# Kernel tuning notes

Hardware: AMD Instinct MI355X
Metric: run time of the kernel (lower is better)

## Reference

```python
import jax, jax.numpy as jnp
import numpy as np

B, N, D, H, FF = 4, 1024, 512, 8, 2048
DH = D // H
RPE_HID = 16
COORD_DIM = 2


def _ln(x, g, b, eps=1e-5):
    m = jnp.mean(x, axis=-1, keepdims=True)
    v = jnp.mean((x - m) ** 2, axis=-1, keepdims=True)
    return (x - m) * jax.lax.rsqrt(v + eps) * g + b


def setup_inputs() -> dict:
    key = jax.random.key(0)
    ks = jax.random.split(key, 20)
    s = 0.02
    inp = {
        "x": jax.random.normal(ks[0], (B, N, D), dtype=jnp.float32),
        "coords": jax.random.uniform(ks[1], (B, N, COORD_DIM), dtype=jnp.float32),
        # qkv + output projections
        "Wq": jax.random.normal(ks[2], (D, D), jnp.float32) * s,
        "bq": jnp.zeros((D,), jnp.float32),
        "Wk": jax.random.normal(ks[3], (D, D), jnp.float32) * s,
        "bk": jnp.zeros((D,), jnp.float32),
        "Wv": jax.random.normal(ks[4], (D, D), jnp.float32) * s,
        "bv": jnp.zeros((D,), jnp.float32),
        "Wo": jax.random.normal(ks[5], (D, D), jnp.float32) * s,
        "bo": jnp.zeros((D,), jnp.float32),
        # learned per-head logit scale (Swin-v2 style cosine attention)
        "logit_scale": jnp.full((H, 1, 1), np.log(10.0), jnp.float32),
        # absolute positional embedder PE: Linear(2 -> D)
        "W_pe": jax.random.normal(ks[6], (COORD_DIM, D), jnp.float32) * s,
        "b_pe": jnp.zeros((D,), jnp.float32),
        # relative positional embedder RPE: MLP(2 -> 16 -> H)
        "W_r1": jax.random.normal(ks[7], (COORD_DIM, RPE_HID), jnp.float32) * 0.5,
        "b_r1": jnp.zeros((RPE_HID,), jnp.float32),
        "W_r2": jax.random.normal(ks[8], (RPE_HID, H), jnp.float32) * 0.5,
        "b_r2": jnp.zeros((H,), jnp.float32),
        # layernorm params
        "g_peq": jnp.ones((D,), jnp.float32), "bt_peq": jnp.zeros((D,), jnp.float32),
        "g_pek": jnp.ones((D,), jnp.float32), "bt_pek": jnp.zeros((D,), jnp.float32),
        "g2": jnp.ones((D,), jnp.float32), "bt2": jnp.zeros((D,), jnp.float32),
        "g3": jnp.ones((D,), jnp.float32), "bt3": jnp.zeros((D,), jnp.float32),
        # MLP (bias=False)
        "W_ff1": jax.random.normal(ks[9], (D, FF), jnp.float32) * s,
        "W_ff2": jax.random.normal(ks[10], (FF, D), jnp.float32) * s,
    }
    return inp


def reference(x, coords, Wq, bq, Wk, bk, Wv, bv, Wo, bo, logit_scale,
              W_pe, b_pe, W_r1, b_r1, W_r2, b_r2,
              g_peq, bt_peq, g_pek, bt_pek, g2, bt2, g3, bt3,
              W_ff1, W_ff2):
    # --- PE add + LayerNorm on q and k (self-attention: coords_cross_ = coords)
    pe = coords @ W_pe + b_pe                      # [B,N,D]
    q = _ln(x + pe, g_peq, bt_peq)
    k = _ln(x + pe, g_pek, bt_pek)
    v = x                                          # v is NOT PE-normed in source

    # --- relative-position bias from cartesian coord differences
    rel = coords[:, :, None, :] - coords[:, None, :, :]   # [B,Nq,Nk,2]
    hid = jax.nn.relu(rel @ W_r1 + b_r1)                  # [B,Nq,Nk,16]
    bias = hid @ W_r2 + b_r2                              # [B,Nq,Nk,H]
    bias = jnp.transpose(bias, (0, 3, 1, 2))              # [B,H,Nq,Nk]

    # --- multi-head cosine attention with learned logit scale
    qp = (q @ Wq + bq).reshape(B, N, H, DH)
    kp = (k @ Wk + bk).reshape(B, N, H, DH)
    vp = (v @ Wv + bv).reshape(B, N, H, DH)
    qn = qp / jnp.maximum(jnp.linalg.norm(qp, axis=-1, keepdims=True), 1e-12)
    kn = kp / jnp.maximum(jnp.linalg.norm(kp, axis=-1, keepdims=True), 1e-12)
    scale = jnp.exp(jnp.minimum(logit_scale, jnp.log(100.0)))  # [H,1,1]
    attn = jnp.einsum('bqhd,bkhd->bhqk', qn, kn) * scale[None] + bias
    attn = jax.nn.softmax(attn, axis=-1)
    att_out = jnp.einsum('bhqk,bkhd->bqhd', attn, vp).reshape(B, N, D)
    att_out = att_out @ Wo + bo

    # --- residual + norm + MLP (LeakyReLU 0.2 after each linear) + residual + norm
    x1 = _ln(x + att_out, g2, bt2)
    mlp = jax.nn.leaky_relu(
        jax.nn.leaky_relu(x1 @ W_ff1, 0.2) @ W_ff2, 0.2)
    return _ln(x1 + mlp, g3, bt3)
```

## Files before the change

### kernel.cpp

```cpp
#include <hip/hip_runtime.h>

#define BB 4
#define NN 1024
#define DD 512
#define HH 8
#define DHH 64
#define FFF 2048

typedef __attribute__((ext_vector_type(8))) short bf16x8;
typedef __attribute__((ext_vector_type(4))) float f32x4;
typedef __attribute__((ext_vector_type(4))) unsigned short u16x4;

__device__ inline float wave_sum(float v) {
#pragma unroll
  for (int off = 32; off; off >>= 1) v += __shfl_xor(v, off);
  return v;
}

__device__ inline unsigned short cvt_bf16(float f) {
  union { float f; unsigned u; } x;
  x.f = f;
  unsigned r = x.u + 0x7FFFu + ((x.u >> 16) & 1u);
  return (unsigned short)(r >> 16);
}

__device__ __forceinline__ void gl_lds16(const void* g, void* l) {
  __builtin_amdgcn_global_load_lds(
      (__attribute__((address_space(1))) void*)(g),
      (__attribute__((address_space(3))) void*)(l), 16, 0, 0);
}

__global__ __launch_bounds__(256) void wconv_kernel(
    const float* __restrict__ W0, const float* __restrict__ W1,
    const float* __restrict__ W2, const float* __restrict__ W3,
    const float* __restrict__ W4, const float* __restrict__ W5,
    unsigned short* __restrict__ out) {
  int bidx = blockIdx.x;
  const float* W; unsigned short* Wt; int K, N, local;
  if (bidx < 256) {
    int sel = bidx >> 6; local = bidx & 63;
    W = sel == 0 ? W0 : sel == 1 ? W1 : sel == 2 ? W2 : W3;
    K = 512; N = 512; Wt = out + (size_t)sel * 262144;
  } else if (bidx < 512) {
    local = bidx - 256; W = W4; K = 512; N = 2048; Wt = out + 1048576;
  } else {
    local = bidx - 512; W = W5; K = 2048; N = 512; Wt = out + 2097152;
  }
  int ntn = N >> 6;
  int tn = (local & (ntn - 1)) << 6, tk = (local / ntn) << 6;
  __shared__ float tile[64][65];
  int tid = threadIdx.x;
#pragma unroll
  for (int i = 0; i < 16; ++i) {
    int e = tid + i * 256, kk = e >> 6, nn = e & 63;
    tile[kk][nn] = W[(size_t)(tk + kk) * N + tn + nn];
  }
  __syncthreads();
#pragma unroll
  for (int i = 0; i < 16; ++i) {
    int e = tid + i * 256, nn = e >> 6, kk = e & 63;
    Wt[(size_t)(tn + nn) * K + tk + kk] = cvt_bf16(tile[kk][nn]);
  }
}

__global__ __launch_bounds__(256) void bias_kernel(
    const float* __restrict__ coords,
    const float* __restrict__ W_r1, const float* __restrict__ b_r1,
    const float* __restrict__ W_r2, const float* __restrict__ b_r2,
    unsigned short* __restrict__ bias_out) {
  int kt = blockIdx.x, qt = blockIdx.y, b = blockIdx.z;
  int tid = threadIdx.x;
  int q = qt * 64 + (tid >> 2);
  int k0 = kt * 32 + (tid & 3) * 8;
  float cq0 = coords[((size_t)b * NN + q) * 2 + 0];
  float cq1 = coords[((size_t)b * NN + q) * 2 + 1];
  float Aq[16];
#pragma unroll
  for (int l = 0; l < 16; ++l)
    Aq[l] = fmaf(cq0, W_r1[l], fmaf(cq1, W_r1[16 + l], b_r1[l]));
  float ck0[8], ck1[8];
#pragma unroll
  for (int kk = 0; kk < 8; ++kk) {
    ck0[kk] = coords[((size_t)b * NN + k0 + kk) * 2 + 0];
    ck1[kk] = coords[((size_t)b * NN + k0 + kk) * 2 + 1];
  }
  float acc[8][8];
#pragma unroll
  for (int kk = 0; kk < 8; ++kk)
#pragma unroll
    for (int h = 0; h < 8; ++h) acc[kk][h] = b_r2[h];
#pragma unroll
  for (int l = 0; l < 16; ++l) {
    float w1a = W_r1[l], w1b = W_r1[16 + l];
#pragma unroll
    for (int kk = 0; kk < 8; ++kk) {
      float hv = Aq[l] - fmaf(ck0[kk], w1a, ck1[kk] * w1b);
      hv = fmaxf(hv, 0.f);
#pragma unroll
      for (int h = 0; h < 8; ++h)
        acc[kk][h] = fmaf(hv, W_r2[l * HH + h], acc[kk][h]);
    }
  }
#pragma unroll
  for (int h = 0; h < 8; ++h) {
    bf16x8 ov;
#pragma unroll
    for (int kk = 0; kk < 8; ++kk) ov[kk] = (short)cvt_bf16(acc[kk][h]);
    *(bf16x8*)&bias_out[(((size_t)b * HH + h) * NN + q) * NN + k0] = ov;
  }
}

__global__ __launch_bounds__(512) void pe_ln_kernel(
    const float* __restrict__ x, const float* __restrict__ coords,
    const float* __restrict__ W_pe, const float* __restrict__ b_pe,
    const float* __restrict__ g_q, const float* __restrict__ bt_q,
    const float* __restrict__ g_k, const float* __restrict__ bt_k,
    unsigned short* __restrict__ q_lnb, unsigned short* __restrict__ k_lnb,
    unsigned short* __restrict__ x_bf) {
  int tid = threadIdx.x;
  int g = tid >> 7, t = tid & 127;
  int row = blockIdx.x * 4 + g;
  int e0 = t * 4;
  float c0 = coords[(size_t)row * 2 + 0];
  float c1 = coords[(size_t)row * 2 + 1];
  size_t base = (size_t)row * DD + e0;
  f32x4 xv = *(const f32x4*)&x[base];
  f32x4 wp0 = *(const f32x4*)&W_pe[e0];
  f32x4 wp1 = *(const f32x4*)&W_pe[DD + e0];
  f32x4 bp  = *(const f32x4*)&b_pe[e0];
  u16x4 xb;
#pragma unroll
  for (int j = 0; j < 4; ++j) xb[j] = cvt_bf16(xv[j]);
  *(u16x4*)&x_bf[base] = xb;
  f32x4 val;
#pragma unroll
  for (int j = 0; j < 4; ++j)
    val[j] = xv[j] + c0 * wp0[j] + c1 * wp1[j] + bp[j];

  __shared__ float ws[8], ws2[8];
  float s = wave_sum(val[0] + val[1] + val[2] + val[3]);
  if ((tid & 63) == 0) ws[tid >> 6] = s;
  __syncthreads();
  float mean = (ws[2 * g] + ws[2 * g + 1]) * (1.f / DD);
  f32x4 dv;
  float s2l = 0.f;
#pragma unroll
  for (int j = 0; j < 4; ++j) { dv[j] = val[j] - mean; s2l = fmaf(dv[j], dv[j], s2l); }
  float s2 = wave_sum(s2l);
  if ((tid & 63) == 0) ws2[tid >> 6] = s2;
  __syncthreads();
  float var = (ws2[2 * g] + ws2[2 * g + 1]) * (1.f / DD);
  float rstd = rsqrtf(var + 1e-5f);
  f32x4 gq = *(const f32x4*)&g_q[e0], bq = *(const f32x4*)&bt_q[e0];
  f32x4 gk = *(const f32x4*)&g_k[e0], bk = *(const f32x4*)&bt_k[e0];
  u16x4 qo, ko;
#pragma unroll
  for (int j = 0; j < 4; ++j) {
    qo[j] = cvt_bf16(dv[j] * rstd * gq[j] + bq[j]);
    ko[j] = cvt_bf16(dv[j] * rstd * gk[j] + bk[j]);
  }
  *(u16x4*)&q_lnb[base] = qo;
  *(u16x4*)&k_lnb[base] = ko;
}

__global__ __launch_bounds__(512) void add_ln_kernel(
    const float* __restrict__ a, const float* __restrict__ r,
    const float* __restrict__ g_, const float* __restrict__ bt,
    float* __restrict__ out, unsigned short* __restrict__ out_bf) {
  int tid = threadIdx.x;
  int g = tid >> 7, t = tid & 127;
  int row = blockIdx.x * 4 + g;
  int e0 = t * 4;
  size_t base = (size_t)row * DD + e0;
  f32x4 av = *(const f32x4*)&a[base];
  f32x4 rv = *(const f32x4*)&r[base];
  f32x4 val;
#pragma unroll
  for (int j = 0; j < 4; ++j) val[j] = av[j] + rv[j];
  __shared__ float ws[8], ws2[8];
  float s = wave_sum(val[0] + val[1] + val[2] + val[3]);
  if ((tid & 63) == 0) ws[tid >> 6] = s;
  __syncthreads();
  float mean = (ws[2 * g] + ws[2 * g + 1]) * (1.f / DD);
  f32x4 dv;
  float s2l = 0.f;
#pragma unroll
  for (int j = 0; j < 4; ++j) { dv[j] = val[j] - mean; s2l = fmaf(dv[j], dv[j], s2l); }
  float s2 = wave_sum(s2l);
  if ((tid & 63) == 0) ws2[tid >> 6] = s2;
  __syncthreads();
  float var = (ws2[2 * g] + ws2[2 * g + 1]) * (1.f / DD);
  float rstd = rsqrtf(var + 1e-5f);
  f32x4 gg = *(const f32x4*)&g_[e0], bb = *(const f32x4*)&bt[e0];
  f32x4 ov;
  u16x4 ob;
#pragma unroll
  for (int j = 0; j < 4; ++j) {
    ov[j] = dv[j] * rstd * gg[j] + bb[j];
    ob[j] = cvt_bf16(ov[j]);
  }
  *(f32x4*)&out[base] = ov;
  if (out_bf) *(u16x4*)&out_bf[base] = ob;
}

template <int ACT, int EPI>
__global__ __launch_bounds__(256) void mgemm_kernel(
    const unsigned short* __restrict__ A, const unsigned short* __restrict__ BT,
    const float* __restrict__ bias, void* __restrict__ C,
    int M, int Nc, int K) {
  __shared__ unsigned short lds[4][8192];
  int tid = threadIdx.x;
  int w = tid >> 6, lane = tid & 63, lg = lane >> 4, lr = lane & 15;
  int bm = blockIdx.y * 128, bn = blockIdx.x * 128;
  int wr = w >> 1, wc = w & 1;
  int segl = lane >> 3;
  int cb = (lane & 7) << 4;

  f32x4 zf = {0.f, 0.f, 0.f, 0.f};
  f32x4 acc[4][4];
#pragma unroll
  for (int mi = 0; mi < 4; ++mi)
#pragma unroll
    for (int ni = 0; ni < 4; ++ni) acc[mi][ni] = zf;

  int nt = K >> 6;

  auto STAGE = [&](int buf, int t) {
    int k0 = t << 6;
#pragma unroll
    for (int i = 0; i < 4; ++i) {
      int seg = w * 4 + i;
      int r = (seg << 3) + segl;
      int csw = cb ^ ((r & 7) << 4);
      const char* ga = (const char*)A + (((size_t)(bm + r) * K + k0) << 1) + csw;
      gl_lds16(ga, &lds[buf * 2][seg << 9]);
      const char* gb = (const char*)BT + (((size_t)(bn + r) * K + k0) << 1) + csw;
      gl_lds16(gb, &lds[buf * 2 + 1][seg << 9]);
    }
  };
  auto COMPUTE = [&](int buf) {
    const unsigned short* As = lds[buf * 2];
    const unsigned short* Bs = lds[buf * 2 + 1];
    bf16x8 af[2][4], bfr[2][4];
#pragma unroll
    for (int kh = 0; kh < 2; ++kh)
#pragma unroll
      for (int mi = 0; mi < 4; ++mi) {
        int r = wr * 64 + mi * 16 + lr;
        int e = (r << 6) + (kh << 5) + (lg << 3);
        af[kh][mi] = *(const bf16x8*)&As[e ^ ((r & 7) << 3)];
        int rb = wc * 64 + mi * 16 + lr;
        int eb = (rb << 6) + (kh << 5) + (lg << 3);
        bfr[kh][mi] = *(const bf16x8*)&Bs[eb ^ ((rb & 7) << 3)];
      }
#pragma unroll
    for (int kh = 0; kh < 2; ++kh)
#pragma unroll
      for (int mi = 0; mi < 4; ++mi)
#pragma unroll
        for (int ni = 0; ni < 4; ++ni)
          acc[mi][ni] = __builtin_amdgcn_mfma_f32_16x16x32_bf16(
              af[kh][mi], bfr[kh][ni], acc[mi][ni], 0, 0, 0);
  };

  STAGE(0, 0);
  __syncthreads();
  for (int t = 0; t < nt; ++t) {
    if (t + 1 < nt) STAGE((t + 1) & 1, t + 1);
    COMPUTE(t & 1);
    __syncthreads();
  }

#pragma unroll
  for (int ni = 0; ni < 4; ++ni) {
    int col = bn + wc * 64 + ni * 16 + lr;
    float bv = bias ? bias[col] : 0.f;
#pragma unroll
    for (int mi = 0; mi < 4; ++mi) {
#pragma unroll
      for (int j = 0; j < 4; ++j) {
        int row = bm + wr * 64 + mi * 16 + lg * 4 + j;
        float v = acc[mi][ni][j] + bv;
        if (ACT == 1) v = v > 0.f ? v : 0.2f * v;
        if (EPI == 1)
          ((unsigned short*)C)[(size_t)row * Nc + col] = cvt_bf16(v);
        else
          ((float*)C)[(size_t)row * Nc + col] = v;
      }
    }
  }
}

template <int ACT, int EPI>
__global__ __launch_bounds__(256) void mgemm64_kernel(
    const unsigned short* __restrict__ A, const unsigned short* __restrict__ BT,
    const float* __restrict__ bias, void* __restrict__ C,
    int M, int Nc, int K) {
  __shared__ unsigned short lds[4][4096];
  int tid = threadIdx.x;
  int w = tid >> 6, lane = tid & 63, lg = lane >> 4, lr = lane & 15;
  int bm = blockIdx.y * 64, bn = blockIdx.x * 64;
  int wr = w >> 1, wc = w & 1;
  int segl = lane >> 3;
  int cb = (lane & 7) << 4;

  f32x4 zf = {0.f, 0.f, 0.f, 0.f};
  f32x4 acc[2][2];
#pragma unroll
  for (int mi = 0; mi < 2; ++mi)
#pragma unroll
    for (int ni = 0; ni < 2; ++ni) acc[mi][ni] = zf;

  int nt = K >> 6;

  auto STAGE = [&](int buf, int t) {
    int k0 = t << 6;
#pragma unroll
    for (int i = 0; i < 2; ++i) {
      int seg = w * 2 + i;
      int r = (seg << 3) + segl;
      int csw = cb ^ ((r & 7) << 4);
      const char* ga = (const char*)A + (((size_t)(bm + r) * K + k0) << 1) + csw;
      gl_lds16(ga, &lds[buf * 2][seg << 9]);
      const char* gb = (const char*)BT + (((size_t)(bn + r) * K + k0) << 1) + csw;
      gl_lds16(gb, &lds[buf * 2 + 1][seg << 9]);
    }
  };
  auto COMPUTE = [&](int buf) {
    const unsigned short* As = lds[buf * 2];
    const unsigned short* Bs = lds[buf * 2 + 1];
    bf16x8 af[2][2], bfr[2][2];
#pragma unroll
    for (int kh = 0; kh < 2; ++kh)
#pragma unroll
      for (int mi = 0; mi < 2; ++mi) {
        int r = wr * 32 + mi * 16 + lr;
        int e = (r << 6) + (kh << 5) + (lg << 3);
        af[kh][mi] = *(const bf16x8*)&As[e ^ ((r & 7) << 3)];
        int rb = wc * 32 + mi * 16 + lr;
        int eb = (rb << 6) + (kh << 5) + (lg << 3);
        bfr[kh][mi] = *(const bf16x8*)&Bs[eb ^ ((rb & 7) << 3)];
      }
#pragma unroll
    for (int kh = 0; kh < 2; ++kh)
#pragma unroll
      for (int mi = 0; mi < 2; ++mi)
#pragma unroll
        for (int ni = 0; ni < 2; ++ni)
          acc[mi][ni] = __builtin_amdgcn_mfma_f32_16x16x32_bf16(
              af[kh][mi], bfr[kh][ni], acc[mi][ni], 0, 0, 0);
  };

  STAGE(0, 0);
  __syncthreads();
  for (int t = 0; t < nt; ++t) {
    if (t + 1 < nt) STAGE((t + 1) & 1, t + 1);
    COMPUTE(t & 1);
    __syncthreads();
  }

#pragma unroll
  for (int ni = 0; ni < 2; ++ni) {
    int col = bn + wc * 32 + ni * 16 + lr;
    float bv = bias ? bias[col] : 0.f;
#pragma unroll
    for (int mi = 0; mi < 2; ++mi) {
#pragma unroll
      for (int j = 0; j < 4; ++j) {
        int row = bm + wr * 32 + mi * 16 + lg * 4 + j;
        float v = acc[mi][ni][j] + bv;
        if (ACT == 1) v = v > 0.f ? v : 0.2f * v;
        if (EPI == 1)
          ((unsigned short*)C)[(size_t)row * Nc + col] = cvt_bf16(v);
        else
          ((float*)C)[(size_t)row * Nc + col] = v;
      }
    }
  }
}

__global__ __launch_bounds__(256) void qkv_gemm_kernel(
    const unsigned short* __restrict__ q_lnb,
    const unsigned short* __restrict__ k_lnb,
    const unsigned short* __restrict__ x_bf,
    const unsigned short* __restrict__ wt,
    const float* __restrict__ bq, const float* __restrict__ bk,
    const float* __restrict__ bv_,
    unsigned short* __restrict__ q_bf, unsigned short* __restrict__ k_bf,
    unsigned short* __restrict__ v_bf) {
  int z = blockIdx.z;
  const unsigned short* A = z == 0 ? q_lnb : z == 1 ? k_lnb : x_bf;
  const unsigned short* BT = wt + (size_t)z * 262144;
  const float* bias = z == 0 ? bq : z == 1 ? bk : bv_;

  __shared__ unsigned short lds[4][8192];
  int tid = threadIdx.x;
  int w = tid >> 6, lane = tid & 63, lg = lane >> 4, lr = lane & 15;
  int bm = blockIdx.y * 128, bn = blockIdx.x * 128;
  int wr = w >> 1, wc = w & 1;
  int segl = lane >> 3;
  int cb = (lane & 7) << 4;

  f32x4 zf = {0.f, 0.f, 0.f, 0.f};
  f32x4 acc[4][4];
#pragma unroll
  for (int mi = 0; mi < 4; ++mi)
#pragma unroll
    for (int ni = 0; ni < 4; ++ni) acc[mi][ni] = zf;

  auto STAGE = [&](int buf, int t) {
    int k0 = t << 6;
#pragma unroll
    for (int i = 0; i < 4; ++i) {
      int seg = w * 4 + i;
      int r = (seg << 3) + segl;
      int csw = cb ^ ((r & 7) << 4);
      const char* ga = (const char*)A + (((size_t)(bm + r) * DD + k0) << 1) + csw;
      gl_lds16(ga, &lds[buf * 2][seg << 9]);
      const char* gb = (const char*)BT + (((size_t)(bn + r) * DD + k0) << 1) + csw;
      gl_lds16(gb, &lds[buf * 2 + 1][seg << 9]);
    }
  };
  auto COMPUTE = [&](int buf) {
    const unsigned short* As = lds[buf * 2];
    const unsigned short* Bs = lds[buf * 2 + 1];
    bf16x8 af[2][4], bfr[2][4];
#pragma unroll
    for (int kh = 0; kh < 2; ++kh)
#pragma unroll
      for (int mi = 0; mi < 4; ++mi) {
        int r = wr * 64 + mi * 16 + lr;
        int e = (r << 6) + (kh << 5) + (lg << 3);
        af[kh][mi] = *(const bf16x8*)&As[e ^ ((r & 7) << 3)];
        int rb = wc * 64 + mi * 16 + lr;
        int eb = (rb << 6) + (kh << 5) + (lg << 3);
        bfr[kh][mi] = *(const bf16x8*)&Bs[eb ^ ((rb & 7) << 3)];
      }
#pragma unroll
    for (int kh = 0; kh < 2; ++kh)
#pragma unroll
      for (int mi = 0; mi < 4; ++mi)
#pragma unroll
        for (int ni = 0; ni < 4; ++ni)
          acc[mi][ni] = __builtin_amdgcn_mfma_f32_16x16x32_bf16(
              af[kh][mi], bfr[kh][ni], acc[mi][ni], 0, 0, 0);
  };

  STAGE(0, 0);
  __syncthreads();
  for (int t = 0; t < 8; ++t) {
    if (t + 1 < 8) STAGE((t + 1) & 1, t + 1);
    COMPUTE(t & 1);
    __syncthreads();
  }

  int h = (bn >> 6) + wc;
  float bvf[4];
#pragma unroll
  for (int ni = 0; ni < 4; ++ni) bvf[ni] = bias[bn + wc * 64 + ni * 16 + lr];
#pragma unroll
  for (int mi = 0; mi < 4; ++mi) {
#pragma unroll
    for (int j = 0; j < 4; ++j) {
      float vals[4]; float ss = 0.f;
#pragma unroll
      for (int ni = 0; ni < 4; ++ni) {
        float v = acc[mi][ni][j] + bvf[ni];
        vals[ni] = v;
        ss = fmaf(v, v, ss);
      }
      float rn = 1.f;
      if (z <= 1) {
        ss += __shfl_xor(ss, 1);
        ss += __shfl_xor(ss, 2);
        ss += __shfl_xor(ss, 4);
        ss += __shfl_xor(ss, 8);
        rn = 1.f / fmaxf(sqrtf(ss), 1e-12f);
      }
      int row = bm + wr * 64 + mi * 16 + lg * 4 + j;
      int b_ = row >> 10, n_ = row & (NN - 1);
      unsigned short* ob = (z == 0 ? q_bf : z == 1 ? k_bf : v_bf) +
                           (((size_t)b_ * HH + h) * NN + n_) * DHH;
#pragma unroll
      for (int ni = 0; ni < 4; ++ni)
        ob[ni * 16 + lr] = cvt_bf16(vals[ni] * rn);
    }
  }
}

template <int NSPLIT>
__global__ __launch_bounds__(256) void attn_kernel(
    const unsigned short* __restrict__ qb, const unsigned short* __restrict__ kb,
    const unsigned short* __restrict__ vb,
    const unsigned short* __restrict__ bias_g,
    const float* __restrict__ logit_scale,
    unsigned short* __restrict__ attb,
    unsigned short* __restrict__ part, int nb) {
  int qt = blockIdx.x, h = blockIdx.y;
  int b = blockIdx.z % nb, sp = blockIdx.z / nb;
  int tid = threadIdx.x;
  int w = tid >> 6, lane = tid & 63;
  int lg = lane >> 4, lr = lane & 15;

  __shared__ unsigned short vt[64 * 64];
  __shared__ unsigned short pl[4][1024];

  const size_t bh = ((size_t)b * HH + h) * NN;
  const int NT = (NN / 64) / NSPLIT;
  const int kt0 = sp * NT;

  int q_glob = qt * 64 + w * 16 + lr;
  bf16x8 aq0 = *(const bf16x8*)&qb[(bh + q_glob) * DHH + lg * 8];
  bf16x8 aq1 = *(const bf16x8*)&qb[(bh + q_glob) * DHH + 32 + lg * 8];

  const unsigned short* brow[4];
#pragma unroll
  for (int r = 0; r < 4; ++r) {
    int qg = qt * 64 + w * 16 + lg * 4 + r;
    brow[r] = &bias_g[(bh + qg) * NN + lr];
  }
  float scale_h = __expf(fminf(logit_scale[h], 4.605170185988091f));

  float m_run[4] = {-1e30f, -1e30f, -1e30f, -1e30f};
  float l_run[4] = {0.f, 0.f, 0.f, 0.f};
  f32x4 zf = {0.f, 0.f, 0.f, 0.f};
  f32x4 acc_o[4] = {zf, zf, zf, zf};

  unsigned short bu[4][4];
#pragma unroll
  for (int r = 0; r < 4; ++r)
#pragma unroll
    for (int kc = 0; kc < 4; ++kc) bu[kc][r] = brow[r][kt0 * 64 + kc * 16];

  for (int t = 0; t < NT; ++t) {
    int ktg = kt0 + t;

    __syncthreads();
#pragma unroll
    for (int it = 0; it < 2; ++it) {
      int kl = it * 32 + (tid & 31);
      int d0 = (tid >> 5) * 8;
      bf16x8 vv = *(const bf16x8*)&vb[(bh + ktg * 64 + kl) * DHH + d0];
#pragma unroll
      for (int j = 0; j < 8; ++j) {
        int d = d0 + j;
        vt[(d * 64 + kl) ^ ((d & 7) << 3)] = (unsigned short)vv[j];
      }
    }
    __syncthreads();

    f32x4 s_acc[4];
#pragma unroll
    for (int kc = 0; kc < 4; ++kc) {
      const unsigned short* krow =
          &kb[(bh + ktg * 64 + kc * 16 + lr) * DHH + lg * 8];
      bf16x8 bk0 = *(const bf16x8*)krow;
      bf16x8 bk1 = *(const bf16x8*)(krow + 32);
      s_acc[kc] = __builtin_amdgcn_mfma_f32_16x16x32_bf16(aq0, bk0, zf, 0, 0, 0);
      s_acc[kc] = __builtin_amdgcn_mfma_f32_16x16x32_bf16(aq1, bk1, s_acc[kc], 0, 0, 0);
    }

#pragma unroll
    for (int kc = 0; kc < 4; ++kc)
#pragma unroll
      for (int r = 0; r < 4; ++r) {
        float bf_ = __uint_as_float(((unsigned)bu[kc][r]) << 16);
        s_acc[kc][r] = fmaf(s_acc[kc][r], scale_h, bf_);
      }

    unsigned short bu2[4][4];
    if (t + 1 < NT) {
#pragma unroll
      for (int r = 0; r < 4; ++r)
#pragma unroll
        for (int kc = 0; kc < 4; ++kc)
          bu2[kc][r] = brow[r][(ktg + 1) * 64 + kc * 16];
    }

    float pf[4][4];
#pragma unroll
    for (int r = 0; r < 4; ++r) {
      float mx = fmaxf(fmaxf(s_acc[0][r], s_acc[1][r]),
                       fmaxf(s_acc[2][r], s_acc[3][r]));
      mx = fmaxf(mx, __shfl_xor(mx, 1));
      mx = fmaxf(mx, __shfl_xor(mx, 2));
      mx = fmaxf(mx, __shfl_xor(mx, 4));
      mx = fmaxf(mx, __shfl_xor(mx, 8));
      float m_new = fmaxf(m_run[r], mx);
      float alpha = __expf(m_run[r] - m_new);
      m_run[r] = m_new;
      float ps = 0.f;
#pragma unroll
      for (int kc = 0; kc < 4; ++kc) {
        float p = __expf(s_acc[kc][r] - m_new);
        pf[kc][r] = p;
        ps += p;
      }
      l_run[r] = l_run[r] * alpha + ps;
#pragma unroll
      for (int ds = 0; ds < 4; ++ds) acc_o[ds][r] *= alpha;
    }

#pragma unroll
    for (int kc = 0; kc < 4; ++kc)
#pragma unroll
      for (int r = 0; r < 4; ++r) {
        int q = lg * 4 + r;
        pl[w][(q * 64 + kc * 16 + lr) ^ ((q & 7) << 3)] = cvt_bf16(pf[kc][r]);
      }

#pragma unroll
    for (int ka = 0; ka < 2; ++ka) {
      bf16x8 pa = *(const bf16x8*)&pl[w][(lr * 64 + ka * 32 + lg * 8) ^
                                         ((lr & 7) << 3)];
#pragma unroll
      for (int ds = 0; ds < 4; ++ds) {
        int d = ds * 16 + lr;
        bf16x8 bv = *(const bf16x8*)&vt[(d * 64 + ka * 32 + lg * 8) ^ ((d & 7) << 3)];
        acc_o[ds] = __builtin_amdgcn_mfma_f32_16x16x32_bf16(pa, bv, acc_o[ds], 0, 0, 0);
      }
    }

    if (t + 1 < NT) {
#pragma unroll
      for (int r = 0; r < 4; ++r)
#pragma unroll
        for (int kc = 0; kc < 4; ++kc) bu[kc][r] = bu2[kc][r];
    }
  }

#pragma unroll
  for (int r = 0; r < 4; ++r) {
    l_run[r] += __shfl_xor(l_run[r], 1);
    l_run[r] += __shfl_xor(l_run[r], 2);
    l_run[r] += __shfl_xor(l_run[r], 4);
    l_run[r] += __shfl_xor(l_run[r], 8);
  }

  if (NSPLIT == 1) {
#pragma unroll
    for (int ds = 0; ds < 4; ++ds)
#pragma unroll
      for (int r = 0; r < 4; ++r) {
        int qg = qt * 64 + w * 16 + lg * 4 + r;
        attb[((size_t)b * NN + qg) * DD + h * DHH + ds * 16 + lr] =
            cvt_bf16(acc_o[ds][r] / l_run[r]);
      }
  } else {
#pragma unroll
    for (int r = 0; r < 4; ++r) {
      int qg = qt * 64 + w * 16 + lg * 4 + r;
      size_t idx = ((size_t)(sp * nb + b) * HH + h) * NN + qg;
      unsigned short* pr = part + idx * 68;
#pragma unroll
      for (int ds = 0; ds < 4; ++ds)
        pr[ds * 16 + lr] = cvt_bf16(acc_o[ds][r]);
      if (lr == 0) {
        *(float*)(pr + 64) = m_run[r];
        *(float*)(pr + 66) = l_run[r];
      }
    }
  }
}

template <int NS>
__global__ __launch_bounds__(256) void combine_kernel(
    const unsigned short* __restrict__ part, unsigned short* __restrict__ attb,
    int nb) {
  int tid = threadIdx.x;
  int w = tid >> 6, d = tid & 63;
  int row = blockIdx.x * 4 + w;
  int b = row >> 13, rem = row & 8191, h = rem >> 10, n = rem & (NN - 1);
  size_t i0 = ((size_t)b * HH + h) * NN + n;
  size_t stride = (size_t)nb * HH * NN;
  float m[NS], l[NS], a[NS];
#pragma unroll
  for (int s = 0; s < NS; ++s) {
    const unsigned short* p = part + (i0 + s * stride) * 68;
    m[s] = *(const float*)(p + 64);
    l[s] = *(const float*)(p + 66);
    a[s] = __uint_as_float(((unsigned)p[d]) << 16);
  }
  float ms = m[0];
#pragma unroll
  for (int s = 1; s < NS; ++s) ms = fmaxf(ms, m[s]);
  float num = 0.f, den = 0.f;
#pragma unroll
  for (int s = 0; s < NS; ++s) {
    float wgt = __expf(m[s] - ms);
    num = fmaf(a[s], wgt, num);
    den = fmaf(l[s], wgt, den);
  }
  attb[((size_t)b * NN + n) * DD + h * DHH + d] = cvt_bf16(num / den);
}

extern "C" void kernel_launch(void* const* d_in, const int* in_sizes, int n_in,
                              void* d_out, int out_size, void* d_ws, size_t ws_size,
                              hipStream_t stream) {
  const float* x      = (const float*)d_in[0];
  const float* coords = (const float*)d_in[1];
  const float* Wq = (const float*)d_in[2];  const float* bq = (const float*)d_in[3];
  const float* Wk = (const float*)d_in[4];  const float* bk = (const float*)d_in[5];
  const float* Wv = (const float*)d_in[6];  const float* bv = (const float*)d_in[7];
  const float* Wo = (const float*)d_in[8];  const float* bo = (const float*)d_in[9];
  const float* logit_scale = (const float*)d_in[10];
  const float* W_pe = (const float*)d_in[11]; const float* b_pe = (const float*)d_in[12];
  const float* W_r1 = (const float*)d_in[13]; const float* b_r1 = (const float*)d_in[14];
  const float* W_r2 = (const float*)d_in[15]; const float* b_r2 = (const float*)d_in[16];
  const float* g_peq = (const float*)d_in[17]; const float* bt_peq = (const float*)d_in[18];
  const float* g_pek = (const float*)d_in[19]; const float* bt_pek = (const float*)d_in[20];
  const float* g2 = (const float*)d_in[21]; const float* bt2 = (const float*)d_in[22];
  const float* g3 = (const float*)d_in[23]; const float* bt3 = (const float*)d_in[24];
  const float* W_ff1 = (const float*)d_in[25];
  const float* W_ff2 = (const float*)d_in[26];
  float* out = (float*)d_out;

  const size_t T = (size_t)BB * NN;
  char* wsb = (char*)d_ws;
  const size_t U = 4u * 1024u * 1024u;

  unsigned short* wt_all = (unsigned short*)(wsb + 0 * U);
  unsigned short* WoT   = wt_all + 786432;
  unsigned short* Wff1T = wt_all + 1048576;
  unsigned short* Wff2T = wt_all + 2097152;
  unsigned short* q_lnb = (unsigned short*)(wsb + 2 * U);
  unsigned short* k_lnb = (unsigned short*)(wsb + 3 * U);
  unsigned short* x_bf  = (unsigned short*)(wsb + 4 * U);
  unsigned short* q_bf  = (unsigned short*)(wsb + 5 * U);
  unsigned short* k_bf  = (unsigned short*)(wsb + 6 * U);
  unsigned short* v_bf  = (unsigned short*)(wsb + 7 * U);
  unsigned short* att_bf = (unsigned short*)(wsb + 8 * U);
  float* proj = (float*)(wsb + 9 * U);
  float* x1   = (float*)(wsb + 11 * U);
  unsigned short* x1_bf = (unsigned short*)(wsb + 13 * U);
  unsigned short* hid_bf = (unsigned short*)(wsb + 2 * U);
  float* mlp  = (float*)(wsb + 9 * U);
  unsigned short* bias_ws = (unsigned short*)(wsb + 9 * U);
  unsigned short* part2_ws = (unsigned short*)(wsb + 2 * U);
  unsigned short* part4_ws = (unsigned short*)(wsb + 25 * U);

  wconv_kernel<<<dim3(768), dim3(256), 0, stream>>>(
      Wq, Wk, Wv, Wo, W_ff1, W_ff2, wt_all);

  pe_ln_kernel<<<dim3(T / 4), dim3(512), 0, stream>>>(
      x, coords, W_pe, b_pe, g_peq, bt_peq, g_pek, bt_pek, q_lnb, k_lnb, x_bf);

  qkv_gemm_kernel<<<dim3(DD / 128, T / 128, 3), dim3(256), 0, stream>>>(
      q_lnb, k_lnb, x_bf, wt_all, bq, bk, bv, q_bf, k_bf, v_bf);

  if (ws_size >= 30 * U) {
    bias_kernel<<<dim3(NN / 32, NN / 64, BB), dim3(256), 0, stream>>>(
        coords, W_r1, b_r1, W_r2, b_r2, bias_ws);
    attn_kernel<4><<<dim3(NN / 64, HH, 4 * BB), dim3(256), 0, stream>>>(
        q_bf, k_bf, v_bf, bias_ws, logit_scale, nullptr, part4_ws, BB);
    combine_kernel<4><<<dim3(BB * HH * NN / 4), dim3(256), 0, stream>>>(
        part4_ws, att_bf, BB);
  } else if (ws_size >= 25 * U) {
    bias_kernel<<<dim3(NN / 32, NN / 64, BB), dim3(256), 0, stream>>>(
        coords, W_r1, b_r1, W_r2, b_r2, bias_ws);
    attn_kernel<2><<<dim3(NN / 64, HH, 2 * BB), dim3(256), 0, stream>>>(
        q_bf, k_bf, v_bf, bias_ws, logit_scale, nullptr, part2_ws, BB);
    combine_kernel<2><<<dim3(BB * HH * NN / 4), dim3(256), 0, stream>>>(
        part2_ws, att_bf, BB);
  } else {
    for (int b = 0; b < BB; ++b) {
      bias_kernel<<<dim3(NN / 32, NN / 64, 1), dim3(256), 0, stream>>>(
          coords + (size_t)b * NN * 2, W_r1, b_r1, W_r2, b_r2, bias_ws);
      attn_kernel<1><<<dim3(NN / 64, HH, 1), dim3(256), 0, stream>>>(
          q_bf + (size_t)b * HH * NN * DHH, k_bf + (size_t)b * HH * NN * DHH,
          v_bf + (size_t)b * HH * NN * DHH, bias_ws, logit_scale,
          att_bf + (size_t)b * NN * DD, nullptr, 1);
    }
  }

  mgemm64_kernel<0, 0><<<dim3(DD / 64, T / 64), dim3(256), 0, stream>>>(
      att_bf, WoT, bo, proj, (int)T, DD, DD);

  add_ln_kernel<<<dim3(T / 4), dim3(512), 0, stream>>>(
      x, proj, g2, bt2, x1, x1_bf);

  mgemm_kernel<1, 1><<<dim3(FFF / 128, T / 128), dim3(256), 0, stream>>>(
      x1_bf, Wff1T, nullptr, hid_bf, (int)T, FFF, DD);
  mgemm64_kernel<1, 0><<<dim3(DD / 64, T / 64), dim3(256), 0, stream>>>(
      hid_bf, Wff2T, nullptr, mlp, (int)T, DD, FFF);

  add_ln_kernel<<<dim3(T / 4), dim3(512), 0, stream>>>(
      x1, mlp, g3, bt3, out, nullptr);
}
```

Before: 170.1 us.

## Replace online softmax with precomputed row-max upper bound and tiled bias/K/V layouts

The bias kernel now also writes per-row partial maxima and stores bias in swizzled 64x64 tiles. The QKV GEMM writes K pre-swizzled and V transposed and swizzled, so attention can bulk-load K, V and bias tiles straight into LDS. Attention uses a fixed upper bound on each row's max (bias max plus scale, since cosine similarity is at most 1), which removes the online rescaling and reduces combine to plain sums. The split grows to 8 ways with 2 tiles per block. It relies on the bound being tight enough that exp does not underflow, and it uses more LDS per block.

```diff
diff --git a/kernel.cpp b/kernel.cpp
--- a/kernel.cpp
+++ b/kernel.cpp
@@ -67,10 +67,11 @@
     const float* __restrict__ coords,
     const float* __restrict__ W_r1, const float* __restrict__ b_r1,
     const float* __restrict__ W_r2, const float* __restrict__ b_r2,
-    unsigned short* __restrict__ bias_out) {
+    unsigned short* __restrict__ bias_out, float* __restrict__ rowmax_out) {
   int kt = blockIdx.x, qt = blockIdx.y, b = blockIdx.z;
   int tid = threadIdx.x;
-  int q = qt * 64 + (tid >> 2);
+  int qL = tid >> 2;
+  int q = qt * 64 + qL;
   int k0 = kt * 32 + (tid & 3) * 8;
   float cq0 = coords[((size_t)b * NN + q) * 2 + 0];
   float cq1 = coords[((size_t)b * NN + q) * 2 + 1];
@@ -101,12 +102,26 @@
         acc[kk][h] = fmaf(hv, W_r2[l * HH + h], acc[kk][h]);
     }
   }
+  int elem = (qL * 64 + (kt & 1) * 32 + (tid & 3) * 8) ^ ((qL & 7) << 3);
+  float mk[8];
 #pragma unroll
   for (int h = 0; h < 8; ++h) {
+    float m = acc[0][h];
+#pragma unroll
+    for (int kk = 1; kk < 8; ++kk) m = fmaxf(m, acc[kk][h]);
+    m = fmaxf(m, __shfl_xor(m, 1));
+    m = fmaxf(m, __shfl_xor(m, 2));
+    mk[h] = m;
     bf16x8 ov;
 #pragma unroll
     for (int kk = 0; kk < 8; ++kk) ov[kk] = (short)cvt_bf16(acc[kk][h]);
-    *(bf16x8*)&bias_out[(((size_t)b * HH + h) * NN + q) * NN + k0] = ov;
+    size_t tile = (((size_t)b * HH + h) * 16 + qt) * 16 + (kt >> 1);
+    *(bf16x8*)&bias_out[tile * 4096 + elem] = ov;
+  }
+  if ((tid & 3) == 0) {
+#pragma unroll
+    for (int h = 0; h < 8; ++h)
+      rowmax_out[(((size_t)b * HH + h) * NN + q) * 32 + kt] = mk[h];
   }
 }
 
@@ -386,8 +401,8 @@
     const unsigned short* __restrict__ wt,
     const float* __restrict__ bq, const float* __restrict__ bk,
     const float* __restrict__ bv_,
-    unsigned short* __restrict__ q_bf, unsigned short* __restrict__ k_bf,
-    unsigned short* __restrict__ v_bf) {
+    unsigned short* __restrict__ q_bf, unsigned short* __restrict__ k_swz,
+    unsigned short* __restrict__ vt_swz) {
   int z = blockIdx.z;
   const unsigned short* A = z == 0 ? q_lnb : z == 1 ? k_lnb : x_bf;
   const unsigned short* BT = wt + (size_t)z * 262144;
@@ -479,22 +494,36 @@
       }
       int row = bm + wr * 64 + mi * 16 + lg * 4 + j;
       int b_ = row >> 10, n_ = row & (NN - 1);
-      unsigned short* ob = (z == 0 ? q_bf : z == 1 ? k_bf : v_bf) +
-                           (((size_t)b_ * HH + h) * NN + n_) * DHH;
-#pragma unroll
-      for (int ni = 0; ni < 4; ++ni)
-        ob[ni * 16 + lr] = cvt_bf16(vals[ni] * rn);
-    }
-  }
-}
-
-template <int NSPLIT>
-__global__ __launch_bounds__(256) void attn_kernel(
+      if (z == 0) {
+        unsigned short* ob = q_bf + (((size_t)b_ * HH + h) * NN + n_) * DHH;
+#pragma unroll
+        for (int ni = 0; ni < 4; ++ni)
+          ob[ni * 16 + lr] = cvt_bf16(vals[ni] * rn);
+      } else if (z == 1) {
+        unsigned short* ob = k_swz + (((size_t)b_ * HH + h) * NN + n_) * DHH;
+#pragma unroll
+        for (int ni = 0; ni < 4; ++ni)
+          ob[(ni * 16 + lr) ^ ((n_ & 7) << 3)] = cvt_bf16(vals[ni] * rn);
+      } else {
+        int ktn = n_ & ~63, nn = n_ & 63;
+#pragma unroll
+        for (int ni = 0; ni < 4; ++ni) {
+          int d = ni * 16 + lr;
+          vt_swz[((size_t)b_ * HH + h) * DHH * NN + (size_t)d * NN + ktn +
+                 (nn ^ ((d & 7) << 3))] = cvt_bf16(vals[ni]);
+        }
+      }
+    }
+  }
+}
+
+template <int NT>
+__global__ __launch_bounds__(256) void attn_vres_kernel(
     const unsigned short* __restrict__ qb, const unsigned short* __restrict__ kb,
-    const unsigned short* __restrict__ vb,
-    const unsigned short* __restrict__ bias_g,
+    const unsigned short* __restrict__ vtg,
+    const unsigned short* __restrict__ bias_t,
+    const float* __restrict__ rowmax_g,
     const float* __restrict__ logit_scale,
-    unsigned short* __restrict__ attb,
     unsigned short* __restrict__ part, int nb) {
   int qt = blockIdx.x, h = blockIdx.y;
   int b = blockIdx.z % nb, sp = blockIdx.z / nb;
@@ -502,60 +531,64 @@
   int w = tid >> 6, lane = tid & 63;
   int lg = lane >> 4, lr = lane & 15;
 
-  __shared__ unsigned short vt[64 * 64];
+  __shared__ unsigned short kl[NT][4096];
+  __shared__ unsigned short vt[NT][4096];
+  __shared__ unsigned short bl[NT][4096];
   __shared__ unsigned short pl[4][1024];
 
   const size_t bh = ((size_t)b * HH + h) * NN;
-  const int NT = (NN / 64) / NSPLIT;
   const int kt0 = sp * NT;
 
   int q_glob = qt * 64 + w * 16 + lr;
   bf16x8 aq0 = *(const bf16x8*)&qb[(bh + q_glob) * DHH + lg * 8];
   bf16x8 aq1 = *(const bf16x8*)&qb[(bh + q_glob) * DHH + 32 + lg * 8];
 
-  const unsigned short* brow[4];
+  float m_ub[4];
+  float scale_h = __expf(fminf(logit_scale[h], 4.605170185988091f));
 #pragma unroll
   for (int r = 0; r < 4; ++r) {
     int qg = qt * 64 + w * 16 + lg * 4 + r;
-    brow[r] = &bias_g[(bh + qg) * NN + lr];
-  }
-  float scale_h = __expf(fminf(logit_scale[h], 4.605170185988091f));
-
-  float m_run[4] = {-1e30f, -1e30f, -1e30f, -1e30f};
+    const float* rmp = &rowmax_g[(bh + qg) * 32];
+    float rm = -1e30f;
+#pragma unroll
+    for (int i = 0; i < 8; ++i) {
+      f32x4 v = *(const f32x4*)&rmp[i * 4];
+      rm = fmaxf(rm, fmaxf(fmaxf(v[0], v[1]), fmaxf(v[2], v[3])));
+    }
+    m_ub[r] = rm + 1.05f * scale_h + 0.1f;
+  }
+
   float l_run[4] = {0.f, 0.f, 0.f, 0.f};
   f32x4 zf = {0.f, 0.f, 0.f, 0.f};
   f32x4 acc_o[4] = {zf, zf, zf, zf};
 
-  unsigned short bu[4][4];
-#pragma unroll
-  for (int r = 0; r < 4; ++r)
-#pragma unroll
-    for (int kc = 0; kc < 4; ++kc) bu[kc][r] = brow[r][kt0 * 64 + kc * 16];
-
+  const unsigned short* kbase = kb + (bh + (size_t)kt0 * 64) * DHH;
+  const unsigned short* bbase =
+      bias_t + ((((size_t)b * HH + h) * 16 + qt) * 16 + kt0) * 4096;
+  const unsigned short* vbase = vtg + ((size_t)b * HH + h) * DHH * NN;
+#pragma unroll
   for (int t = 0; t < NT; ++t) {
-    int ktg = kt0 + t;
-
-    __syncthreads();
-#pragma unroll
-    for (int it = 0; it < 2; ++it) {
-      int kl = it * 32 + (tid & 31);
-      int d0 = (tid >> 5) * 8;
-      bf16x8 vv = *(const bf16x8*)&vb[(bh + ktg * 64 + kl) * DHH + d0];
-#pragma unroll
-      for (int j = 0; j < 8; ++j) {
-        int d = d0 + j;
-        vt[(d * 64 + kl) ^ ((d & 7) << 3)] = (unsigned short)vv[j];
-      }
-    }
-    __syncthreads();
-
+#pragma unroll
+    for (int i = 0; i < 2; ++i) {
+      int chunk = i * 256 + w * 64;
+      int idx = chunk + lane;
+      gl_lds16(kbase + (size_t)t * 4096 + (size_t)idx * 8, &kl[t][chunk * 8]);
+      gl_lds16(bbase + (size_t)t * 4096 + (size_t)idx * 8, &bl[t][chunk * 8]);
+      int d = idx >> 3, kc8 = (idx & 7) * 8;
+      gl_lds16(vbase + (size_t)d * NN + (kt0 + t) * 64 + kc8,
+               &vt[t][chunk * 8]);
+    }
+  }
+  __syncthreads();
+
+  for (int t = 0; t < NT; ++t) {
     f32x4 s_acc[4];
 #pragma unroll
     for (int kc = 0; kc < 4; ++kc) {
-      const unsigned short* krow =
-          &kb[(bh + ktg * 64 + kc * 16 + lr) * DHH + lg * 8];
-      bf16x8 bk0 = *(const bf16x8*)krow;
-      bf16x8 bk1 = *(const bf16x8*)(krow + 32);
+      int row = kc * 16 + lr;
+      int sw = (row & 7) << 3;
+      bf16x8 bk0 = *(const bf16x8*)&kl[t][row * 64 + ((lg * 8) ^ sw)];
+      bf16x8 bk1 = *(const bf16x8*)&kl[t][row * 64 + ((32 + lg * 8) ^ sw)];
       s_acc[kc] = __builtin_amdgcn_mfma_f32_16x16x32_bf16(aq0, bk0, zf, 0, 0, 0);
       s_acc[kc] = __builtin_amdgcn_mfma_f32_16x16x32_bf16(aq1, bk1, s_acc[kc], 0, 0, 0);
     }
@@ -564,49 +597,14 @@
     for (int kc = 0; kc < 4; ++kc)
 #pragma unroll
       for (int r = 0; r < 4; ++r) {
-        float bf_ = __uint_as_float(((unsigned)bu[kc][r]) << 16);
-        s_acc[kc][r] = fmaf(s_acc[kc][r], scale_h, bf_);
-      }
-
-    unsigned short bu2[4][4];
-    if (t + 1 < NT) {
-#pragma unroll
-      for (int r = 0; r < 4; ++r)
-#pragma unroll
-        for (int kc = 0; kc < 4; ++kc)
-          bu2[kc][r] = brow[r][(ktg + 1) * 64 + kc * 16];
-    }
-
-    float pf[4][4];
-#pragma unroll
-    for (int r = 0; r < 4; ++r) {
-      float mx = fmaxf(fmaxf(s_acc[0][r], s_acc[1][r]),
-                       fmaxf(s_acc[2][r], s_acc[3][r]));
-      mx = fmaxf(mx, __shfl_xor(mx, 1));
-      mx = fmaxf(mx, __shfl_xor(mx, 2));
-      mx = fmaxf(mx, __shfl_xor(mx, 4));
-      mx = fmaxf(mx, __shfl_xor(mx, 8));
-      float m_new = fmaxf(m_run[r], mx);
-      float alpha = __expf(m_run[r] - m_new);
-      m_run[r] = m_new;
-      float ps = 0.f;
-#pragma unroll
-      for (int kc = 0; kc < 4; ++kc) {
-        float p = __expf(s_acc[kc][r] - m_new);
-        pf[kc][r] = p;
-        ps += p;
-      }
-      l_run[r] = l_run[r] * alpha + ps;
-#pragma unroll
-      for (int ds = 0; ds < 4; ++ds) acc_o[ds][r] *= alpha;
-    }
-
-#pragma unroll
-    for (int kc = 0; kc < 4; ++kc)
-#pragma unroll
-      for (int r = 0; r < 4; ++r) {
-        int q = lg * 4 + r;
-        pl[w][(q * 64 + kc * 16 + lr) ^ ((q & 7) << 3)] = cvt_bf16(pf[kc][r]);
+        int q = w * 16 + lg * 4 + r;
+        unsigned short ub =
+            bl[t][(q * 64 + kc * 16 + lr) ^ ((q & 7) << 3)];
+        float bf_ = __uint_as_float(((unsigned)ub) << 16);
+        float p = __expf(fmaf(s_acc[kc][r], scale_h, bf_ - m_ub[r]));
+        l_run[r] += p;
+        int ql = lg * 4 + r;
+        pl[w][(ql * 64 + kc * 16 + lr) ^ ((ql & 7) << 3)] = cvt_bf16(p);
       }
 
 #pragma unroll
@@ -616,16 +614,10 @@
 #pragma unroll
       for (int ds = 0; ds < 4; ++ds) {
         int d = ds * 16 + lr;
-        bf16x8 bv = *(const bf16x8*)&vt[(d * 64 + ka * 32 + lg * 8) ^ ((d & 7) << 3)];
+        bf16x8 bv = *(const bf16x8*)&vt[t][(d * 64 + ka * 32 + lg * 8) ^
+                                           ((d & 7) << 3)];
         acc_o[ds] = __builtin_amdgcn_mfma_f32_16x16x32_bf16(pa, bv, acc_o[ds], 0, 0, 0);
       }
-    }
-
-    if (t + 1 < NT) {
-#pragma unroll
-      for (int r = 0; r < 4; ++r)
-#pragma unroll
-        for (int kc = 0; kc < 4; ++kc) bu[kc][r] = bu2[kc][r];
     }
   }
 
@@ -637,29 +629,15 @@
     l_run[r] += __shfl_xor(l_run[r], 8);
   }
 
-  if (NSPLIT == 1) {
+#pragma unroll
+  for (int r = 0; r < 4; ++r) {
+    int qg = qt * 64 + w * 16 + lg * 4 + r;
+    size_t idx = ((size_t)(sp * nb + b) * HH + h) * NN + qg;
+    unsigned short* pr = part + idx * 68;
 #pragma unroll
     for (int ds = 0; ds < 4; ++ds)
-#pragma unroll
-      for (int r = 0; r < 4; ++r) {
-        int qg = qt * 64 + w * 16 + lg * 4 + r;
-        attb[((size_t)b * NN + qg) * DD + h * DHH + ds * 16 + lr] =
-            cvt_bf16(acc_o[ds][r] / l_run[r]);
-      }
-  } else {
-#pragma unroll
-    for (int r = 0; r < 4; ++r) {
-      int qg = qt * 64 + w * 16 + lg * 4 + r;
-      size_t idx = ((size_t)(sp * nb + b) * HH + h) * NN + qg;
-      unsigned short* pr = part + idx * 68;
-#pragma unroll
-      for (int ds = 0; ds < 4; ++ds)
-        pr[ds * 16 + lr] = cvt_bf16(acc_o[ds][r]);
-      if (lr == 0) {
-        *(float*)(pr + 64) = m_run[r];
-        *(float*)(pr + 66) = l_run[r];
-      }
-    }
+      pr[ds * 16 + lr] = cvt_bf16(acc_o[ds][r]);
+    if (lr == 0) *(float*)(pr + 64) = l_run[r];
   }
 }
 
@@ -673,23 +651,12 @@
   int b = row >> 13, rem = row & 8191, h = rem >> 10, n = rem & (NN - 1);
   size_t i0 = ((size_t)b * HH + h) * NN + n;
   size_t stride = (size_t)nb * HH * NN;
-  float m[NS], l[NS], a[NS];
+  float num = 0.f, den = 0.f;
 #pragma unroll
   for (int s = 0; s < NS; ++s) {
     const unsigned short* p = part + (i0 + s * stride) * 68;
-    m[s] = *(const float*)(p + 64);
-    l[s] = *(const float*)(p + 66);
-    a[s] = __uint_as_float(((unsigned)p[d]) << 16);
-  }
-  float ms = m[0];
-#pragma unroll
-  for (int s = 1; s < NS; ++s) ms = fmaxf(ms, m[s]);
-  float num = 0.f, den = 0.f;
-#pragma unroll
-  for (int s = 0; s < NS; ++s) {
-    float wgt = __expf(m[s] - ms);
-    num = fmaf(a[s], wgt, num);
-    den = fmaf(l[s], wgt, den);
+    num += __uint_as_float(((unsigned)p[d]) << 16);
+    den += *(const float*)(p + 64);
   }
   attb[((size_t)b * NN + n) * DD + h * DHH + d] = cvt_bf16(num / den);
 }
@@ -727,17 +694,17 @@
   unsigned short* k_lnb = (unsigned short*)(wsb + 3 * U);
   unsigned short* x_bf  = (unsigned short*)(wsb + 4 * U);
   unsigned short* q_bf  = (unsigned short*)(wsb + 5 * U);
-  unsigned short* k_bf  = (unsigned short*)(wsb + 6 * U);
-  unsigned short* v_bf  = (unsigned short*)(wsb + 7 * U);
+  unsigned short* k_swz = (unsigned short*)(wsb + 6 * U);
+  unsigned short* v_swz = (unsigned short*)(wsb + 7 * U);
   unsigned short* att_bf = (unsigned short*)(wsb + 8 * U);
   float* proj = (float*)(wsb + 9 * U);
   float* x1   = (float*)(wsb + 11 * U);
   unsigned short* x1_bf = (unsigned short*)(wsb + 13 * U);
   unsigned short* hid_bf = (unsigned short*)(wsb + 2 * U);
   float* mlp  = (float*)(wsb + 9 * U);
+  float* rowmax_ws = (float*)(wsb + 2 * U);
   unsigned short* bias_ws = (unsigned short*)(wsb + 9 * U);
-  unsigned short* part2_ws = (unsigned short*)(wsb + 2 * U);
-  unsigned short* part4_ws = (unsigned short*)(wsb + 25 * U);
+  unsigned short* part_ws = (unsigned short*)(wsb + 25 * U);
 
   wconv_kernel<<<dim3(768), dim3(256), 0, stream>>>(
       Wq, Wk, Wv, Wo, W_ff1, W_ff2, wt_all);
@@ -746,30 +713,28 @@
       x, coords, W_pe, b_pe, g_peq, bt_peq, g_pek, bt_pek, q_lnb, k_lnb, x_bf);
 
   qkv_gemm_kernel<<<dim3(DD / 128, T / 128, 3), dim3(256), 0, stream>>>(
-      q_lnb, k_lnb, x_bf, wt_all, bq, bk, bv, q_bf, k_bf, v_bf);
-
-  if (ws_size >= 30 * U) {
+      q_lnb, k_lnb, x_bf, wt_all, bq, bk, bv, q_bf, k_swz, v_swz);
+
+  if (ws_size >= 34 * U) {
     bias_kernel<<<dim3(NN / 32, NN / 64, BB), dim3(256), 0, stream>>>(
-        coords, W_r1, b_r1, W_r2, b_r2, bias_ws);
-    attn_kernel<4><<<dim3(NN / 64, HH, 4 * BB), dim3(256), 0, stream>>>(
-        q_bf, k_bf, v_bf, bias_ws, logit_scale, nullptr, part4_ws, BB);
-    combine_kernel<4><<<dim3(BB * HH * NN / 4), dim3(256), 0, stream>>>(
-        part4_ws, att_bf, BB);
-  } else if (ws_size >= 25 * U) {
-    bias_kernel<<<dim3(NN / 32, NN / 64, BB), dim3(256), 0, stream>>>(
-        coords, W_r1, b_r1, W_r2, b_r2, bias_ws);
-    attn_kernel<2><<<dim3(NN / 64, HH, 2 * BB), dim3(256), 0, stream>>>(
-        q_bf, k_bf, v_bf, bias_ws, logit_scale, nullptr, part2_ws, BB);
-    combine_kernel<2><<<dim3(BB * HH * NN / 4), dim3(256), 0, stream>>>(
-        part2_ws, att_bf, BB);
+        coords, W_r1, b_r1, W_r2, b_r2, bias_ws, rowmax_ws);
+    attn_vres_kernel<2><<<dim3(NN / 64, HH, 8 * BB), dim3(256), 0, stream>>>(
+        q_bf, k_swz, v_swz, bias_ws, rowmax_ws, logit_scale, part_ws, BB);
+    combine_kernel<8><<<dim3(BB * HH * NN / 4), dim3(256), 0, stream>>>(
+        part_ws, att_bf, BB);
   } else {
+    unsigned short* bias_b = (unsigned short*)(wsb + 9 * U);
+    unsigned short* part_b = (unsigned short*)(wsb + 13 * U);
+    float* rm_b = (float*)(wsb + 2 * U);
     for (int b = 0; b < BB; ++b) {
       bias_kernel<<<dim3(NN / 32, NN / 64, 1), dim3(256), 0, stream>>>(
-          coords + (size_t)b * NN * 2, W_r1, b_r1, W_r2, b_r2, bias_ws);
-      attn_kernel<1><<<dim3(NN / 64, HH, 1), dim3(256), 0, stream>>>(
-          q_bf + (size_t)b * HH * NN * DHH, k_bf + (size_t)b * HH * NN * DHH,
-          v_bf + (size_t)b * HH * NN * DHH, bias_ws, logit_scale,
-          att_bf + (size_t)b * NN * DD, nullptr, 1);
+          coords + (size_t)b * NN * 2, W_r1, b_r1, W_r2, b_r2, bias_b, rm_b);
+      attn_vres_kernel<2><<<dim3(NN / 64, HH, 8), dim3(256), 0, stream>>>(
+          q_bf + (size_t)b * HH * NN * DHH, k_swz + (size_t)b * HH * NN * DHH,
+          v_swz + (size_t)b * HH * DHH * NN, bias_b, rm_b, logit_scale,
+          part_b, 1);
+      combine_kernel<8><<<dim3(HH * NN / 4), dim3(256), 0, stream>>>(
+          part_b, att_bf + (size_t)b * NN * DD, 1);
     }
   }
 
```

Result: slower. 178.6 us (+5.0%).
